# Kernel optimization log

Hardware: AMD Instinct MI355X
Metric: run time of the kernel (lower is better)

The kernel has to match this reference:

```python
import jax, jax.numpy as jnp
import numpy as np

B, T, X, H, NU, NODE, HL = 256, 200, 128, 512, 100, 100, 512

def _lin(k, nin, nout):
    kw, kb = jax.random.split(k)
    s = 1.0 / np.sqrt(nin).astype(np.float32)
    return (jax.random.uniform(kw, (nin, nout), jnp.float32, -s, s),
            jax.random.uniform(kb, (nout,), jnp.float32, -s, s))

def setup_inputs() -> dict:
    key = jax.random.key(0)
    ks = jax.random.split(key, 16)
    d = {}
    d['x_data'] = jax.random.normal(ks[0], (B, T, X), jnp.float32)
    d['x_time'] = jnp.linspace(0.0, 1.0, T, dtype=jnp.float32)
    cin = 2 * H + X
    d['Wu1'], d['bu1'] = _lin(ks[1], cin, NU)
    d['Wu2'], d['bu2'] = _lin(ks[2], NU, H)
    d['Wr1'], d['br1'] = _lin(ks[3], cin, NU)
    d['Wr2'], d['br2'] = _lin(ks[4], NU, H)
    d['Wn1'], d['bn1'] = _lin(ks[5], cin, NU)
    d['Wn2'], d['bn2'] = _lin(ks[6], NU, 2 * H)
    d['Wo1'], d['bo1'] = _lin(ks[7], H, NODE)
    d['Wo2'], d['bo2'] = _lin(ks[8], NODE, H)
    d['Wt1'], d['bt1'] = _lin(ks[9], 2 * H, 100)
    d['Wt2'], d['bt2'] = _lin(ks[10], 100, 100)
    d['Wt3'], d['bt3'] = _lin(ks[11], 100, 2 * HL)
    return d

def reference(x_data, x_time, Wu1, bu1, Wu2, bu2, Wr1, br1, Wr2, br2,
              Wn1, bn1, Wn2, bn2, Wo1, bo1, Wo2, bo2,
              Wt1, bt1, Wt2, bt2, Wt3, bt3):
    b, t, _ = x_data.shape
    h_dim = Wu2.shape[1]

    def ode_f(h):  # diff_func: MLP h -> tanh -> h (time-independent)
        return jnp.tanh(h @ Wo1 + bo1) @ Wo2 + bo2

    def gru(h, hs, x):  # GRU_with_std update
        yc = jnp.concatenate([h, hs, x], -1)
        u = jax.nn.sigmoid(jnp.tanh(yc @ Wu1 + bu1) @ Wu2 + bu2)
        r = jax.nn.sigmoid(jnp.tanh(yc @ Wr1 + br1) @ Wr2 + br2)
        c = jnp.concatenate([h * r, hs * r, x], -1)
        ns = jnp.tanh(c @ Wn1 + bn1) @ Wn2 + bn2
        m, s = ns[:, :h_dim], jnp.abs(ns[:, h_dim:])
        return (1.0 - u) * m + u * h, (1.0 - u) * s + u * hs

    # dt sequence replicating the torch loop's (prev_ti, ti) bookkeeping;
    # all |dt gaps| < minimum_step so the Euler branch is always taken.
    dts = jnp.concatenate([jnp.full((1,), -0.01, x_time.dtype),
                           (x_time[-1] - x_time[0])[None],
                           x_time[:-2] - x_time[1:-1]])
    xs = jnp.swapaxes(x_data, 0, 1)  # (T, B, X)

    def step(carry, inp):
        h, hs = carry
        x_t, dt = inp
        h_ode = h + dt * ode_f(h)          # single Euler ODE step
        h2, hs2 = gru(h_ode, hs, x_t)      # GRU update (no NaNs in data)
        return (h2, hs2), None

    h0 = jnp.zeros((b, h_dim), x_data.dtype)
    (hT, hsT), _ = jax.lax.scan(step, (h0, h0), (xs, dts))

    # run_to_prior tail: transform_h_last then split / abs
    hcat = jnp.concatenate([hT[None], hsT[None]], -1)  # (1, B, 2H)
    z = jnp.tanh(hcat @ Wt1 + bt1)
    z = jnp.tanh(z @ Wt2 + bt2)
    z = z @ Wt3 + bt3
    hl = z.shape[-1] // 2
    mu, sigma = z[..., :hl], jnp.abs(z[..., hl:])
    return mu, sigma
```

## Files before the change

### kernel.cpp

```cpp
#include <hip/hip_runtime.h>

typedef unsigned short ushort_t;
typedef _Float16 half_t;
typedef __attribute__((ext_vector_type(8))) _Float16 half8;
typedef __attribute__((ext_vector_type(4))) float f32x4;

#define B_ 256
#define T_ 200
#define X_ 128
#define H_ 512

#define OFF_WO1 0
#define OFF_WO2 57344
#define OFF_WU1 122880
#define OFF_WR1 251904
#define OFF_WN1 380928
#define OFF_WU2 509952
#define OFF_WR2 575488
#define OFF_WN2 641024
#define OFF_WT1 772096
#define OFF_WT2 886784
#define OFF_WT3 901120
#define SWZ_TOTAL 1032192
#define DTS_BYTE_OFF (SWZ_TOTAL * 2)

#define LOG2E 1.4426950408889634f


struct Args {
  const float *x_data, *x_time;
  const float *Wu1, *bu1, *Wu2, *bu2;
  const float *Wr1, *br1, *Wr2, *br2;
  const float *Wn1, *bn1, *Wn2, *bn2;
  const float *Wo1, *bo1, *Wo2, *bo2;
  const float *Wt1, *bt1, *Wt2, *bt2, *Wt3, *bt3;
  float* out;
  half_t* wsw;
  float* dts;
};

__device__ __forceinline__ float fast_sigm(float x) {
  return __builtin_amdgcn_rcpf(1.0f + __builtin_amdgcn_exp2f(-LOG2E * x));
}
__device__ __forceinline__ float fast_tanh(float x) {
  return 1.0f - 2.0f * __builtin_amdgcn_rcpf(1.0f + __builtin_amdgcn_exp2f((2.0f * LOG2E) * x));
}

template <int KB>
__device__ __forceinline__ f32x4 gemm_tile(const half_t* __restrict__ wtile,
                                           const half_t* __restrict__ abase,
                                           int astride, int lane, f32x4 acc) {
  const half_t* ap = abase + (lane & 15) * astride + 8 * (lane >> 4);
  const half_t* wp = wtile + lane * 8;
#pragma unroll 4
  for (int kb = 0; kb < KB; ++kb) {
    half8 af = *(const half8*)(ap + kb * 32);
    half8 bf = *(const half8*)(wp + kb * 512);
    acc = __builtin_amdgcn_mfma_f32_16x16x32_f16(af, bf, acc, 0, 0, 0);
  }
  return acc;
}

template <int KB>
__device__ __forceinline__ void gemm_tile2(const half_t* __restrict__ w0,
                                           const half_t* __restrict__ w1,
                                           const half_t* __restrict__ abase,
                                           int astride, int lane,
                                           f32x4& acc0, f32x4& acc1) {
  const half_t* ap = abase + (lane & 15) * astride + 8 * (lane >> 4);
  const half_t* wp0 = w0 + lane * 8;
  const half_t* wp1 = w1 + lane * 8;
#pragma unroll 2
  for (int kb = 0; kb < KB; ++kb) {
    half8 af = *(const half8*)(ap + kb * 32);
    half8 b0 = *(const half8*)(wp0 + kb * 512);
    half8 b1 = *(const half8*)(wp1 + kb * 512);
    acc0 = __builtin_amdgcn_mfma_f32_16x16x32_f16(af, b0, acc0, 0, 0, 0);
    acc1 = __builtin_amdgcn_mfma_f32_16x16x32_f16(af, b1, acc1, 0, 0, 0);
  }
}

__global__ void swz_kernel(Args a) {
  struct WT { const float* src; int off; int KB; int Kr; int Nr; };
  const WT tbl[11] = {
      {a.Wo1, OFF_WO1, 16, 512, 100},  {a.Wo2, OFF_WO2, 4, 100, 512},
      {a.Wu1, OFF_WU1, 36, 1152, 100}, {a.Wr1, OFF_WR1, 36, 1152, 100},
      {a.Wn1, OFF_WN1, 36, 1152, 100}, {a.Wu2, OFF_WU2, 4, 100, 512},
      {a.Wr2, OFF_WR2, 4, 100, 512},   {a.Wn2, OFF_WN2, 4, 100, 1024},
      {a.Wt1, OFF_WT1, 32, 1024, 100}, {a.Wt2, OFF_WT2, 4, 100, 100},
      {a.Wt3, OFF_WT3, 4, 100, 1024}};
  const int ends[11] = {OFF_WO2, OFF_WU1, OFF_WR1, OFF_WN1, OFF_WU2, OFF_WR2,
                        OFF_WN2, OFF_WT1, OFF_WT2, OFF_WT3, SWZ_TOTAL};
  int gid = blockIdx.x * blockDim.x + threadIdx.x;
  int e8 = gid * 8;
  if (e8 >= SWZ_TOTAL) return;
  int w = 0;
  while (e8 >= ends[w]) ++w;
  const WT T = tbl[w];
  int local = e8 - T.off;
  int lane = (local >> 3) & 63;
  int blk = local >> 9;
  int kb = blk % T.KB, nt = blk / T.KB;
  int n = nt * 16 + (lane & 15);
  int k0 = kb * 32 + 8 * (lane >> 4);
#pragma unroll
  for (int j = 0; j < 8; ++j) {
    int k = k0 + j;
    float v = (k < T.Kr && n < T.Nr) ? T.src[k * T.Nr + n] : 0.0f;
    a.wsw[e8 + j] = (half_t)v;
  }
}

__global__ void dts_kernel(Args a) {
  int t = threadIdx.x;
  if (t >= T_) return;
  float v;
  if (t == 0)      v = -0.01f;
  else if (t == 1) v = a.x_time[T_ - 1] - a.x_time[0];
  else             v = a.x_time[t - 2] - a.x_time[t - 1];
  a.dts[t] = v;
}

__global__ __launch_bounds__(1024) void odegru_kernel(Args a) {
  __shared__ __align__(16) half_t yc[16 * 1160];
  __shared__ __align__(16) half_t tg[16 * 136];
  __shared__ __align__(16) half_t tu[16 * 136];
  __shared__ __align__(16) half_t tr[16 * 136];
  __shared__ __align__(16) half_t tn[16 * 136];
  __shared__ float dts_s[T_];

  const int tid = threadIdx.x;
  const int wave = tid >> 6;
  const int lane = tid & 63;
  const int lm = lane & 15;
  const int g = lane >> 4;
  const int row0 = blockIdx.x * 16;

  for (int i = tid; i < 16 * 136; i += 1024) {
    tg[i] = (half_t)0.f; tu[i] = (half_t)0.f; tr[i] = (half_t)0.f; tn[i] = (half_t)0.f;
  }
  if (tid < T_) dts_s[tid] = a.dts[tid];

  const int xm = tid >> 7, xk = tid & 127;
  const float* xb0 = a.x_data + (long)(row0 + xm) * T_ * X_ + xk;
  const float* xb1 = xb0 + (long)8 * T_ * X_;
  float xp0 = xb0[0];
  float xp1 = xb1[0];

  float hreg[8], hsreg[8];
#pragma unroll
  for (int i = 0; i < 8; ++i) { hreg[i] = 0.f; hsreg[i] = 0.f; }
  float ureg[8];
  __syncthreads();

  for (int t = 0; t < T_; ++t) {
    const float dt = dts_s[t];
#pragma unroll
    for (int s = 0; s < 2; ++s) {
      int n = (wave + s * 16) * 16 + lm;
#pragma unroll
      for (int i = 0; i < 4; ++i) {
        int m = g * 4 + i;
        yc[m * 1160 + n]       = (half_t)hreg[s * 4 + i];
        yc[m * 1160 + 512 + n] = (half_t)hsreg[s * 4 + i];
      }
    }
    yc[xm * 1160 + 1024 + xk]       = (half_t)xp0;
    yc[(xm + 8) * 1160 + 1024 + xk] = (half_t)xp1;
    __syncthreads();
    if (t + 1 < T_) {
      xp0 = xb0[(t + 1) * X_];
      xp1 = xb1[(t + 1) * X_];
    }
    for (int nt = wave; nt < 7; nt += 16) {
      f32x4 acc = {0.f, 0.f, 0.f, 0.f};
      acc = gemm_tile<16>(a.wsw + OFF_WO1 + nt * 16 * 512, yc, 1160, lane, acc);
      int n = nt * 16 + lm;
      if (n < 100) {
        float bias = a.bo1[n];
#pragma unroll
        for (int i = 0; i < 4; ++i)
          tg[(g * 4 + i) * 136 + n] = (half_t)fast_tanh(acc[i] + bias);
      }
    }
    __syncthreads();
    {
      f32x4 acc0 = {0.f, 0.f, 0.f, 0.f}, acc1 = {0.f, 0.f, 0.f, 0.f};
      gemm_tile2<4>(a.wsw + OFF_WO2 + wave * 4 * 512,
                    a.wsw + OFF_WO2 + (wave + 16) * 4 * 512,
                    tg, 136, lane, acc0, acc1);
#pragma unroll
      for (int s = 0; s < 2; ++s) {
        const f32x4& acc = s ? acc1 : acc0;
        int n = (wave + s * 16) * 16 + lm;
        float bias = a.bo2[n];
#pragma unroll
        for (int i = 0; i < 4; ++i) {
          int m = g * 4 + i;
          float h_ode = hreg[s * 4 + i] + dt * (acc[i] + bias);
          hreg[s * 4 + i] = h_ode;
          yc[m * 1160 + n] = (half_t)h_ode;
        }
      }
    }
    __syncthreads();
    for (int nt = wave; nt < 14; nt += 16) {
      bool isU = nt < 7;
      int nt7 = isU ? nt : nt - 7;
      f32x4 acc = {0.f, 0.f, 0.f, 0.f};
      acc = gemm_tile<36>(a.wsw + (isU ? OFF_WU1 : OFF_WR1) + nt7 * 36 * 512, yc, 1160, lane, acc);
      int n = nt7 * 16 + lm;
      if (n < 100) {
        float bias = (isU ? a.bu1 : a.br1)[n];
        half_t* dst = isU ? tu : tr;
#pragma unroll
        for (int i = 0; i < 4; ++i)
          dst[(g * 4 + i) * 136 + n] = (half_t)fast_tanh(acc[i] + bias);
      }
    }
    __syncthreads();
    {
      f32x4 acc0 = {0.f, 0.f, 0.f, 0.f}, acc1 = {0.f, 0.f, 0.f, 0.f};
      gemm_tile2<4>(a.wsw + OFF_WU2 + wave * 4 * 512,
                    a.wsw + OFF_WU2 + (wave + 16) * 4 * 512,
                    tu, 136, lane, acc0, acc1);
#pragma unroll
      for (int s = 0; s < 2; ++s) {
        const f32x4& acc = s ? acc1 : acc0;
        int n = (wave + s * 16) * 16 + lm;
        float bias = a.bu2[n];
#pragma unroll
        for (int i = 0; i < 4; ++i) ureg[s * 4 + i] = fast_sigm(acc[i] + bias);
      }
    }
    {
      f32x4 acc0 = {0.f, 0.f, 0.f, 0.f}, acc1 = {0.f, 0.f, 0.f, 0.f};
      gemm_tile2<4>(a.wsw + OFF_WR2 + wave * 4 * 512,
                    a.wsw + OFF_WR2 + (wave + 16) * 4 * 512,
                    tr, 136, lane, acc0, acc1);
#pragma unroll
      for (int s = 0; s < 2; ++s) {
        const f32x4& acc = s ? acc1 : acc0;
        int n = (wave + s * 16) * 16 + lm;
        float bias = a.br2[n];
#pragma unroll
        for (int i = 0; i < 4; ++i) {
          int m = g * 4 + i;
          float r = fast_sigm(acc[i] + bias);
          yc[m * 1160 + n]       = (half_t)(hreg[s * 4 + i] * r);
          yc[m * 1160 + 512 + n] = (half_t)(hsreg[s * 4 + i] * r);
        }
      }
    }
    __syncthreads();
    for (int nt = wave; nt < 7; nt += 16) {
      f32x4 acc = {0.f, 0.f, 0.f, 0.f};
      acc = gemm_tile<36>(a.wsw + OFF_WN1 + nt * 36 * 512, yc, 1160, lane, acc);
      int n = nt * 16 + lm;
      if (n < 100) {
        float bias = a.bn1[n];
#pragma unroll
        for (int i = 0; i < 4; ++i)
          tn[(g * 4 + i) * 136 + n] = (half_t)fast_tanh(acc[i] + bias);
      }
    }
    __syncthreads();
    {
      f32x4 acc0 = {0.f, 0.f, 0.f, 0.f}, acc1 = {0.f, 0.f, 0.f, 0.f};
      gemm_tile2<4>(a.wsw + OFF_WN2 + wave * 4 * 512,
                    a.wsw + OFF_WN2 + (wave + 16) * 4 * 512,
                    tn, 136, lane, acc0, acc1);
#pragma unroll
      for (int s = 0; s < 2; ++s) {
        const f32x4& acc = s ? acc1 : acc0;
        int n = (wave + s * 16) * 16 + lm;
        float bias = a.bn2[n];
#pragma unroll
        for (int i = 0; i < 4; ++i) {
          float u = ureg[s * 4 + i];
          float mval = acc[i] + bias;
          hreg[s * 4 + i] = (1.0f - u) * mval + u * hreg[s * 4 + i];
        }
      }
    }
    {
      f32x4 acc0 = {0.f, 0.f, 0.f, 0.f}, acc1 = {0.f, 0.f, 0.f, 0.f};
      gemm_tile2<4>(a.wsw + OFF_WN2 + (wave + 32) * 4 * 512,
                    a.wsw + OFF_WN2 + (wave + 48) * 4 * 512,
                    tn, 136, lane, acc0, acc1);
#pragma unroll
      for (int s = 0; s < 2; ++s) {
        const f32x4& acc = s ? acc1 : acc0;
        int n = (wave + 32 + s * 16) * 16 + lm;
        float bias = a.bn2[n];
#pragma unroll
        for (int i = 0; i < 4; ++i) {
          float u = ureg[s * 4 + i];
          float sval = fabsf(acc[i] + bias);
          hsreg[s * 4 + i] = (1.0f - u) * sval + u * hsreg[s * 4 + i];
        }
      }
    }
  }

#pragma unroll
  for (int s = 0; s < 2; ++s) {
    int n = (wave + s * 16) * 16 + lm;
#pragma unroll
    for (int i = 0; i < 4; ++i) {
      int m = g * 4 + i;
      yc[m * 1160 + n]       = (half_t)hreg[s * 4 + i];
      yc[m * 1160 + 512 + n] = (half_t)hsreg[s * 4 + i];
    }
  }
  __syncthreads();
  for (int nt = wave; nt < 7; nt += 16) {
    f32x4 acc = {0.f, 0.f, 0.f, 0.f};
    acc = gemm_tile<32>(a.wsw + OFF_WT1 + nt * 32 * 512, yc, 1160, lane, acc);
    int n = nt * 16 + lm;
    if (n < 100) {
      float bias = a.bt1[n];
#pragma unroll
      for (int i = 0; i < 4; ++i)
        tu[(g * 4 + i) * 136 + n] = (half_t)fast_tanh(acc[i] + bias);
    }
  }
  __syncthreads();
  for (int nt = wave; nt < 7; nt += 16) {
    f32x4 acc = {0.f, 0.f, 0.f, 0.f};
    acc = gemm_tile<4>(a.wsw + OFF_WT2 + nt * 4 * 512, tu, 136, lane, acc);
    int n = nt * 16 + lm;
    if (n < 100) {
      float bias = a.bt2[n];
#pragma unroll
      for (int i = 0; i < 4; ++i)
        tr[(g * 4 + i) * 136 + n] = (half_t)fast_tanh(acc[i] + bias);
    }
  }
  __syncthreads();
#pragma unroll
  for (int s = 0; s < 4; ++s) {
    int nt = wave + s * 16;
    f32x4 acc = {0.f, 0.f, 0.f, 0.f};
    acc = gemm_tile<4>(a.wsw + OFF_WT3 + nt * 4 * 512, tr, 136, lane, acc);
    int n = nt * 16 + lm;
    float bias = a.bt3[n];
#pragma unroll
    for (int i = 0; i < 4; ++i) {
      int grow = row0 + g * 4 + i;
      float val = acc[i] + bias;
      if (n < 512)
        a.out[(size_t)grow * 512 + n] = val;
      else
        a.out[(size_t)(B_ * 512) + (size_t)grow * 512 + (n - 512)] = fabsf(val);
    }
  }
}

extern "C" void kernel_launch(void* const* d_in, const int* in_sizes, int n_in,
                              void* d_out, int out_size, void* d_ws, size_t ws_size,
                              hipStream_t stream) {
  Args a;
  a.x_data = (const float*)d_in[0];
  a.x_time = (const float*)d_in[1];
  a.Wu1 = (const float*)d_in[2];  a.bu1 = (const float*)d_in[3];
  a.Wu2 = (const float*)d_in[4];  a.bu2 = (const float*)d_in[5];
  a.Wr1 = (const float*)d_in[6];  a.br1 = (const float*)d_in[7];
  a.Wr2 = (const float*)d_in[8];  a.br2 = (const float*)d_in[9];
  a.Wn1 = (const float*)d_in[10]; a.bn1 = (const float*)d_in[11];
  a.Wn2 = (const float*)d_in[12]; a.bn2 = (const float*)d_in[13];
  a.Wo1 = (const float*)d_in[14]; a.bo1 = (const float*)d_in[15];
  a.Wo2 = (const float*)d_in[16]; a.bo2 = (const float*)d_in[17];
  a.Wt1 = (const float*)d_in[18]; a.bt1 = (const float*)d_in[19];
  a.Wt2 = (const float*)d_in[20]; a.bt2 = (const float*)d_in[21];
  a.Wt3 = (const float*)d_in[22]; a.bt3 = (const float*)d_in[23];
  a.out = (float*)d_out;
  a.wsw = (half_t*)d_ws;
  a.dts = (float*)((char*)d_ws + DTS_BYTE_OFF);

  swz_kernel<<<dim3(504), dim3(256), 0, stream>>>(a);
  dts_kernel<<<dim3(1), dim3(256), 0, stream>>>(a);
  odegru_kernel<<<dim3(16), dim3(1024), 0, stream>>>(a);
}
```

Baseline: 2.875 ms.

## Overlap u/r gate partial GEMM over hs and x with ODE first layer

The hs and x parts of the u and r first-layer GEMMs (K chunks 16..35) do not depend on the Euler-updated h. They are now computed as 28 partial pieces during the Wo1 phase, when only 7 of 16 waves were busy. The partials are stored in a new fp32 shared buffer, and the later u/r GEMM only processes the h part (16 K-chunks), starting from the summed partials. This balances wave load and shortens the serial critical path, at the cost of extra shared memory and a changed accumulation order.

```diff
diff --git a/kernel.cpp b/kernel.cpp
--- a/kernel.cpp
+++ b/kernel.cpp
@@ -127,6 +127,7 @@
   __shared__ __align__(16) half_t tu[16 * 136];
   __shared__ __align__(16) half_t tr[16 * 136];
   __shared__ __align__(16) half_t tn[16 * 136];
+  __shared__ __align__(16) float pur[28 * 272];
   __shared__ float dts_s[T_];
 
   const int tid = threadIdx.x;
@@ -153,6 +154,19 @@
   float ureg[8];
   __syncthreads();
 
+  auto do_piece = [&](int p) {
+    int t2 = p >> 1, half = p & 1;
+    bool isU = t2 < 7;
+    int nt7 = isU ? t2 : t2 - 7;
+    f32x4 acc = {0.f, 0.f, 0.f, 0.f};
+    acc = gemm_tile<10>(
+        a.wsw + (isU ? OFF_WU1 : OFF_WR1) + nt7 * 36 * 512 + (16 + 10 * half) * 512,
+        yc + 512 + half * 320, 1160, lane, acc);
+#pragma unroll
+    for (int i = 0; i < 4; ++i)
+      pur[p * 272 + (g * 4 + i) * 17 + lm] = acc[i];
+  };
+
   for (int t = 0; t < T_; ++t) {
     const float dt = dts_s[t];
 #pragma unroll
@@ -172,16 +186,22 @@
       xp0 = xb0[(t + 1) * X_];
       xp1 = xb1[(t + 1) * X_];
     }
-    for (int nt = wave; nt < 7; nt += 16) {
+    if (wave < 7) {
       f32x4 acc = {0.f, 0.f, 0.f, 0.f};
-      acc = gemm_tile<16>(a.wsw + OFF_WO1 + nt * 16 * 512, yc, 1160, lane, acc);
-      int n = nt * 16 + lm;
+      acc = gemm_tile<16>(a.wsw + OFF_WO1 + wave * 16 * 512, yc, 1160, lane, acc);
+      int n = wave * 16 + lm;
       if (n < 100) {
         float bias = a.bo1[n];
 #pragma unroll
         for (int i = 0; i < 4; ++i)
           tg[(g * 4 + i) * 136 + n] = (half_t)fast_tanh(acc[i] + bias);
       }
+      do_piece(wave);
+    } else {
+      int j = wave - 7;
+      int p0 = j < 3 ? 7 + j * 3 : 16 + (j - 3) * 2;
+      int cnt = j < 3 ? 3 : 2;
+      for (int k = 0; k < cnt; ++k) do_piece(p0 + k);
     }
     __syncthreads();
     {
@@ -207,8 +227,13 @@
     for (int nt = wave; nt < 14; nt += 16) {
       bool isU = nt < 7;
       int nt7 = isU ? nt : nt - 7;
-      f32x4 acc = {0.f, 0.f, 0.f, 0.f};
-      acc = gemm_tile<36>(a.wsw + (isU ? OFF_WU1 : OFF_WR1) + nt7 * 36 * 512, yc, 1160, lane, acc);
+      f32x4 acc;
+#pragma unroll
+      for (int i = 0; i < 4; ++i)
+        acc[i] = pur[(2 * nt) * 272 + (g * 4 + i) * 17 + lm] +
+                 pur[(2 * nt + 1) * 272 + (g * 4 + i) * 17 + lm];
+      acc = gemm_tile<16>(a.wsw + (isU ? OFF_WU1 : OFF_WR1) + nt7 * 36 * 512,
+                          yc, 1160, lane, acc);
       int n = nt7 * 16 + lm;
       if (n < 100) {
         float bias = (isU ? a.bu1 : a.br1)[n];
```

Result: slower. 3.500 ms (+21.7%).
